# Performance work log

Measured on AMD Instinct MI355X. Metric: run time of the kernel, lower is better.

Reference implementation:

```python
import jax, jax.numpy as jnp
import numpy as np
from jax import lax

TIMESTEPS = 10
KSIZE = 2
STRIDE = 2


def setup_inputs() -> dict:
    key = jax.random.key(0)
    k1, _ = jax.random.split(key)
    x = jax.random.normal(k1, (32, 96, 128, 128), dtype=jnp.float32)
    # torch init: np.full((1, C, 1, 1), 0.1)
    pool_strength = jnp.ones((1, 96, 1, 1), dtype=jnp.float32) * 0.1
    return {"x": x, "pool_strength": pool_strength}


def _maxpool3x3_same(x):
    # MaxPool2d(kernel=3, stride=1, padding=1) on NCHW
    return lax.reduce_window(
        x, -jnp.inf, lax.max,
        window_dimensions=(1, 1, 3, 3),
        window_strides=(1, 1, 1, 1),
        padding=((0, 0), (0, 0), (1, 1), (1, 1)))


def reference(x, pool_strength):
    def step(cur, _):
        pooled = _maxpool3x3_same(cur)
        cur = cur + pool_strength * (pooled - cur)
        return cur, None

    cur, _ = lax.scan(step, x, None, length=TIMESTEPS)
    # AvgPool2d(kernel=2, stride=2, padding=0)
    s = lax.reduce_window(
        cur, 0.0, lax.add,
        window_dimensions=(1, 1, KSIZE, KSIZE),
        window_strides=(1, 1, STRIDE, STRIDE),
        padding='VALID')
    return s / float(KSIZE * KSIZE)
```

## Files before the change

kernel.cpp:

```cpp
#include <hip/hip_runtime.h>
#include <math.h>


#define TSTEPS 10
#define PW 128
#define PH 128
#define HPITCH 132

__device__ __forceinline__ float dpp_recv_left(float x) {
    int r = __builtin_amdgcn_update_dpp((int)0xff800000, __float_as_int(x),
                                        0x111, 0xf, 0xf, false);
    return __int_as_float(r);
}
__device__ __forceinline__ float dpp_recv_right(float x) {
    int r = __builtin_amdgcn_update_dpp((int)0xff800000, __float_as_int(x),
                                        0x101, 0xf, 0xf, false);
    return __int_as_float(r);
}

__device__ __forceinline__ float max3f(float a, float b, float c) {
    return fmaxf(fmaxf(a, b), c);
}

__device__ __forceinline__ void hmax_row(const float* v, float* h) {
    float vl = dpp_recv_left(v[7]);
    float vr = dpp_recv_right(v[0]);
    h[0] = max3f(vl, v[0], v[1]);
#pragma unroll
    for (int c = 1; c < 7; ++c) h[c] = max3f(v[c-1], v[c], v[c+1]);
    h[7] = max3f(v[6], v[7], vr);
}

__global__ __launch_bounds__(256, 3)
void cpool_kernel(const float* __restrict__ x, const float* __restrict__ ps,
                  float* __restrict__ out) {
    __shared__ float hbuf[32 * HPITCH];

    const int b  = blockIdx.x;
    const int ch = b % 96;
    const float p = ps[ch];

    const int tid = threadIdx.x;
    const int tx = tid & 15;
    const int ty = tid >> 4;
    const int x0 = tx << 3;
    const int y0 = ty << 3;

    const float* __restrict__ xp = x + (size_t)b * (PH * PW);

    float cur[8][8];
#pragma unroll
    for (int r = 0; r < 8; ++r) {
        const float4 a  = *(const float4*)(xp + (y0 + r) * PW + x0);
        const float4 bq = *(const float4*)(xp + (y0 + r) * PW + x0 + 4);
        cur[r][0] = a.x;  cur[r][1] = a.y;  cur[r][2] = a.z;  cur[r][3] = a.w;
        cur[r][4] = bq.x; cur[r][5] = bq.y; cur[r][6] = bq.z; cur[r][7] = bq.w;
    }

    const float NEG = -__builtin_huge_valf();

#pragma unroll 1
    for (int t = 0; t < TSTEPS; ++t) {
        float hTop[8], hBot[8];
        hmax_row(cur[0], hTop);
        hmax_row(cur[7], hBot);

        *(float4*)&hbuf[(2*ty)   * HPITCH + x0]     = make_float4(hTop[0], hTop[1], hTop[2], hTop[3]);
        *(float4*)&hbuf[(2*ty)   * HPITCH + x0 + 4] = make_float4(hTop[4], hTop[5], hTop[6], hTop[7]);
        *(float4*)&hbuf[(2*ty+1) * HPITCH + x0]     = make_float4(hBot[0], hBot[1], hBot[2], hBot[3]);
        *(float4*)&hbuf[(2*ty+1) * HPITCH + x0 + 4] = make_float4(hBot[4], hBot[5], hBot[6], hBot[7]);

        __syncthreads();

        float hm[8], hnx[8];
        if (ty > 0) {
            float4 a  = *(const float4*)&hbuf[(2*ty - 1) * HPITCH + x0];
            float4 bq = *(const float4*)&hbuf[(2*ty - 1) * HPITCH + x0 + 4];
            hm[0] = a.x;  hm[1] = a.y;  hm[2] = a.z;  hm[3] = a.w;
            hm[4] = bq.x; hm[5] = bq.y; hm[6] = bq.z; hm[7] = bq.w;
        } else {
#pragma unroll
            for (int c = 0; c < 8; ++c) hm[c] = NEG;
        }
        if (ty < 15) {
            float4 a  = *(const float4*)&hbuf[(2*ty + 2) * HPITCH + x0];
            float4 bq = *(const float4*)&hbuf[(2*ty + 2) * HPITCH + x0 + 4];
            hnx[0] = a.x;  hnx[1] = a.y;  hnx[2] = a.z;  hnx[3] = a.w;
            hnx[4] = bq.x; hnx[5] = bq.y; hnx[6] = bq.z; hnx[7] = bq.w;
        } else {
#pragma unroll
            for (int c = 0; c < 8; ++c) hnx[c] = NEG;
        }

        float hc[8];
#pragma unroll
        for (int c = 0; c < 8; ++c) hc[c] = hTop[c];

#pragma unroll
        for (int r = 0; r < 8; ++r) {
            float hn[8];
            if (r < 6) {
                hmax_row(cur[r + 1], hn);
            } else if (r == 6) {
#pragma unroll
                for (int c = 0; c < 8; ++c) hn[c] = hBot[c];
            } else {
#pragma unroll
                for (int c = 0; c < 8; ++c) hn[c] = hnx[c];
            }
#pragma unroll
            for (int c = 0; c < 8; ++c) {
                float v = max3f(hm[c], hc[c], hn[c]);
                cur[r][c] = fmaf(p, v - cur[r][c], cur[r][c]);
            }
#pragma unroll
            for (int c = 0; c < 8; ++c) { hm[c] = hc[c]; hc[c] = hn[c]; }
        }

        __syncthreads();
    }

    float* __restrict__ op = out + (size_t)b * (64 * 64);
#pragma unroll
    for (int r2 = 0; r2 < 4; ++r2) {
        float4 o;
        o.x = 0.25f * (cur[2*r2][0] + cur[2*r2][1] + cur[2*r2+1][0] + cur[2*r2+1][1]);
        o.y = 0.25f * (cur[2*r2][2] + cur[2*r2][3] + cur[2*r2+1][2] + cur[2*r2+1][3]);
        o.z = 0.25f * (cur[2*r2][4] + cur[2*r2][5] + cur[2*r2+1][4] + cur[2*r2+1][5]);
        o.w = 0.25f * (cur[2*r2][6] + cur[2*r2][7] + cur[2*r2+1][6] + cur[2*r2+1][7]);
        *(float4*)(op + (size_t)((ty * 4 + r2) * 64 + tx * 4)) = o;
    }
}

extern "C" void kernel_launch(void* const* d_in, const int* in_sizes, int n_in,
                              void* d_out, int out_size, void* d_ws, size_t ws_size,
                              hipStream_t stream) {
    const float* x  = (const float*)d_in[0];
    const float* ps = (const float*)d_in[1];
    float* out = (float*)d_out;
    (void)in_sizes; (void)n_in; (void)out_size; (void)d_ws; (void)ws_size;

    cpool_kernel<<<dim3(32 * 96), dim3(256), 0, stream>>>(x, ps, out);
}
```

Baseline: 300.0 us.

## Use 512 threads with 4x8 tiles and double-buffered halo exchange

```diff
diff --git a/kernel.cpp b/kernel.cpp
--- a/kernel.cpp
+++ b/kernel.cpp
@@ -1,18 +1,17 @@
 #include <hip/hip_runtime.h>
-#include <math.h>
 
 
 #define TSTEPS 10
 #define PW 128
-#define PH 128
-#define HPITCH 132
+#define HP 132
+#define HROWS 31
 
-__device__ __forceinline__ float dpp_recv_left(float x) {
+__device__ __forceinline__ float dpp_left(float x) {
     int r = __builtin_amdgcn_update_dpp((int)0xff800000, __float_as_int(x),
                                         0x111, 0xf, 0xf, false);
     return __int_as_float(r);
 }
-__device__ __forceinline__ float dpp_recv_right(float x) {
+__device__ __forceinline__ float dpp_right(float x) {
     int r = __builtin_amdgcn_update_dpp((int)0xff800000, __float_as_int(x),
                                         0x101, 0xf, 0xf, false);
     return __int_as_float(r);
@@ -23,112 +22,113 @@
 }
 
 __device__ __forceinline__ void hmax_row(const float* v, float* h) {
-    float vl = dpp_recv_left(v[7]);
-    float vr = dpp_recv_right(v[0]);
+    float vl = dpp_left(v[7]);
+    float vr = dpp_right(v[0]);
     h[0] = max3f(vl, v[0], v[1]);
 #pragma unroll
-    for (int c = 1; c < 7; ++c) h[c] = max3f(v[c-1], v[c], v[c+1]);
+    for (int c = 1; c < 7; ++c) h[c] = max3f(v[c - 1], v[c], v[c + 1]);
     h[7] = max3f(v[6], v[7], vr);
 }
 
-__global__ __launch_bounds__(256, 3)
+__device__ __forceinline__ void ld8(const float* a, float* d) {
+    float4 u = ((const float4*)a)[0], v = ((const float4*)a)[1];
+    d[0] = u.x; d[1] = u.y; d[2] = u.z; d[3] = u.w;
+    d[4] = v.x; d[5] = v.y; d[6] = v.z; d[7] = v.w;
+}
+__device__ __forceinline__ void st8(float* a, const float* d) {
+    ((float4*)a)[0] = make_float4(d[0], d[1], d[2], d[3]);
+    ((float4*)a)[1] = make_float4(d[4], d[5], d[6], d[7]);
+}
+
+__device__ __forceinline__ void do_step(float cur[4][8], float p, int tx, int ty,
+                                        float* __restrict__ topBuf,
+                                        float* __restrict__ botBuf) {
+    const float NEG = -__builtin_huge_valf();
+    const int x0 = tx * 8;
+
+    float hTop[8], hBot[8];
+    hmax_row(cur[0], hTop);
+    hmax_row(cur[3], hBot);
+
+    if (ty > 0)  st8(topBuf + (ty - 1) * HP + x0, hTop);
+    if (ty < 31) st8(botBuf + ty * HP + x0, hBot);
+
+    __syncthreads();
+
+    float hm[8], hnx[8];
+    if (ty > 0) {
+        ld8(botBuf + (ty - 1) * HP + x0, hm);
+    } else {
+#pragma unroll
+        for (int c = 0; c < 8; ++c) hm[c] = NEG;
+    }
+    if (ty < 31) {
+        ld8(topBuf + ty * HP + x0, hnx);
+    } else {
+#pragma unroll
+        for (int c = 0; c < 8; ++c) hnx[c] = NEG;
+    }
+
+    float hc[8];
+#pragma unroll
+    for (int c = 0; c < 8; ++c) hc[c] = hTop[c];
+
+#pragma unroll
+    for (int r = 0; r < 4; ++r) {
+        float hn[8];
+        if (r < 2) {
+            hmax_row(cur[r + 1], hn);
+        } else if (r == 2) {
+#pragma unroll
+            for (int c = 0; c < 8; ++c) hn[c] = hBot[c];
+        } else {
+#pragma unroll
+            for (int c = 0; c < 8; ++c) hn[c] = hnx[c];
+        }
+#pragma unroll
+        for (int c = 0; c < 8; ++c) {
+            float v = max3f(hm[c], hc[c], hn[c]);
+            cur[r][c] = fmaf(p, v - cur[r][c], cur[r][c]);
+        }
+#pragma unroll
+        for (int c = 0; c < 8; ++c) { hm[c] = hc[c]; hc[c] = hn[c]; }
+    }
+}
+
+__global__ __launch_bounds__(512, 4)
 void cpool_kernel(const float* __restrict__ x, const float* __restrict__ ps,
                   float* __restrict__ out) {
-    __shared__ float hbuf[32 * HPITCH];
+    __shared__ float lds[2][2][HROWS * HP];
 
-    const int b  = blockIdx.x;
-    const int ch = b % 96;
-    const float p = ps[ch];
+    const int b = blockIdx.x;
+    const float p = ps[b % 96];
 
-    const int tid = threadIdx.x;
-    const int tx = tid & 15;
-    const int ty = tid >> 4;
-    const int x0 = tx << 3;
-    const int y0 = ty << 3;
+    const int tx = threadIdx.x & 15;
+    const int ty = threadIdx.x >> 4;
+    const int x0 = tx * 8;
+    const int y0 = ty * 4;
 
-    const float* __restrict__ xp = x + (size_t)b * (PH * PW);
+    const float* __restrict__ xp = x + (size_t)b * (PW * PW);
 
-    float cur[8][8];
+    float cur[4][8];
 #pragma unroll
-    for (int r = 0; r < 8; ++r) {
-        const float4 a  = *(const float4*)(xp + (y0 + r) * PW + x0);
-        const float4 bq = *(const float4*)(xp + (y0 + r) * PW + x0 + 4);
-        cur[r][0] = a.x;  cur[r][1] = a.y;  cur[r][2] = a.z;  cur[r][3] = a.w;
-        cur[r][4] = bq.x; cur[r][5] = bq.y; cur[r][6] = bq.z; cur[r][7] = bq.w;
-    }
-
-    const float NEG = -__builtin_huge_valf();
+    for (int r = 0; r < 4; ++r) ld8(xp + (y0 + r) * PW + x0, cur[r]);
 
 #pragma unroll 1
-    for (int t = 0; t < TSTEPS; ++t) {
-        float hTop[8], hBot[8];
-        hmax_row(cur[0], hTop);
-        hmax_row(cur[7], hBot);
-
-        *(float4*)&hbuf[(2*ty)   * HPITCH + x0]     = make_float4(hTop[0], hTop[1], hTop[2], hTop[3]);
-        *(float4*)&hbuf[(2*ty)   * HPITCH + x0 + 4] = make_float4(hTop[4], hTop[5], hTop[6], hTop[7]);
-        *(float4*)&hbuf[(2*ty+1) * HPITCH + x0]     = make_float4(hBot[0], hBot[1], hBot[2], hBot[3]);
-        *(float4*)&hbuf[(2*ty+1) * HPITCH + x0 + 4] = make_float4(hBot[4], hBot[5], hBot[6], hBot[7]);
-
-        __syncthreads();
-
-        float hm[8], hnx[8];
-        if (ty > 0) {
-            float4 a  = *(const float4*)&hbuf[(2*ty - 1) * HPITCH + x0];
-            float4 bq = *(const float4*)&hbuf[(2*ty - 1) * HPITCH + x0 + 4];
-            hm[0] = a.x;  hm[1] = a.y;  hm[2] = a.z;  hm[3] = a.w;
-            hm[4] = bq.x; hm[5] = bq.y; hm[6] = bq.z; hm[7] = bq.w;
-        } else {
-#pragma unroll
-            for (int c = 0; c < 8; ++c) hm[c] = NEG;
-        }
-        if (ty < 15) {
-            float4 a  = *(const float4*)&hbuf[(2*ty + 2) * HPITCH + x0];
-            float4 bq = *(const float4*)&hbuf[(2*ty + 2) * HPITCH + x0 + 4];
-            hnx[0] = a.x;  hnx[1] = a.y;  hnx[2] = a.z;  hnx[3] = a.w;
-            hnx[4] = bq.x; hnx[5] = bq.y; hnx[6] = bq.z; hnx[7] = bq.w;
-        } else {
-#pragma unroll
-            for (int c = 0; c < 8; ++c) hnx[c] = NEG;
-        }
-
-        float hc[8];
-#pragma unroll
-        for (int c = 0; c < 8; ++c) hc[c] = hTop[c];
-
-#pragma unroll
-        for (int r = 0; r < 8; ++r) {
-            float hn[8];
-            if (r < 6) {
-                hmax_row(cur[r + 1], hn);
-            } else if (r == 6) {
-#pragma unroll
-                for (int c = 0; c < 8; ++c) hn[c] = hBot[c];
-            } else {
-#pragma unroll
-                for (int c = 0; c < 8; ++c) hn[c] = hnx[c];
-            }
-#pragma unroll
-            for (int c = 0; c < 8; ++c) {
-                float v = max3f(hm[c], hc[c], hn[c]);
-                cur[r][c] = fmaf(p, v - cur[r][c], cur[r][c]);
-            }
-#pragma unroll
-            for (int c = 0; c < 8; ++c) { hm[c] = hc[c]; hc[c] = hn[c]; }
-        }
-
-        __syncthreads();
+    for (int tt = 0; tt < TSTEPS / 2; ++tt) {
+        do_step(cur, p, tx, ty, lds[0][0], lds[0][1]);
+        do_step(cur, p, tx, ty, lds[1][0], lds[1][1]);
     }
 
     float* __restrict__ op = out + (size_t)b * (64 * 64);
 #pragma unroll
-    for (int r2 = 0; r2 < 4; ++r2) {
+    for (int r2 = 0; r2 < 2; ++r2) {
         float4 o;
         o.x = 0.25f * (cur[2*r2][0] + cur[2*r2][1] + cur[2*r2+1][0] + cur[2*r2+1][1]);
         o.y = 0.25f * (cur[2*r2][2] + cur[2*r2][3] + cur[2*r2+1][2] + cur[2*r2+1][3]);
         o.z = 0.25f * (cur[2*r2][4] + cur[2*r2][5] + cur[2*r2+1][4] + cur[2*r2+1][5]);
         o.w = 0.25f * (cur[2*r2][6] + cur[2*r2][7] + cur[2*r2+1][6] + cur[2*r2+1][7]);
-        *(float4*)(op + (size_t)((ty * 4 + r2) * 64 + tx * 4)) = o;
+        *(float4*)(op + (size_t)((2 * ty + r2) * 64 + tx * 4)) = o;
     }
 }
 
@@ -140,5 +140,5 @@
     float* out = (float*)d_out;
     (void)in_sizes; (void)n_in; (void)out_size; (void)d_ws; (void)ws_size;
 
-    cpool_kernel<<<dim3(32 * 96), dim3(256), 0, stream>>>(x, ps, out);
+    cpool_kernel<<<dim3(32 * 96), dim3(512), 0, stream>>>(x, ps, out);
 }
```

Result: faster. 292.9 us (-2.4%).

## Replace shared-memory halo exchange with per-wave redundant row bands

Applied to the files above, without the earlier changes.

```diff
diff --git a/kernel.cpp b/kernel.cpp
--- a/kernel.cpp
+++ b/kernel.cpp
@@ -1,20 +1,17 @@
 #include <hip/hip_runtime.h>
-#include <math.h>
 
 
+#define PW 128
 #define TSTEPS 10
-#define PW 128
-#define PH 128
-#define HPITCH 132
 
-__device__ __forceinline__ float dpp_recv_left(float x) {
+__device__ __forceinline__ float dpp_wave_left(float x) {
     int r = __builtin_amdgcn_update_dpp((int)0xff800000, __float_as_int(x),
-                                        0x111, 0xf, 0xf, false);
+                                        0x138, 0xf, 0xf, false);
     return __int_as_float(r);
 }
-__device__ __forceinline__ float dpp_recv_right(float x) {
+__device__ __forceinline__ float dpp_wave_right(float x) {
     int r = __builtin_amdgcn_update_dpp((int)0xff800000, __float_as_int(x),
-                                        0x101, 0xf, 0xf, false);
+                                        0x130, 0xf, 0xf, false);
     return __int_as_float(r);
 }
 
@@ -22,113 +19,78 @@
     return fmaxf(fmaxf(a, b), c);
 }
 
-__device__ __forceinline__ void hmax_row(const float* v, float* h) {
-    float vl = dpp_recv_left(v[7]);
-    float vr = dpp_recv_right(v[0]);
-    h[0] = max3f(vl, v[0], v[1]);
+template<int NROWS, int RS0>
+__device__ __forceinline__ void run_band(const float* __restrict__ xp,
+                                         float* __restrict__ op,
+                                         float p, int lane, int row_base,
+                                         int out_row0)
+{
+    float c0[NROWS], c1[NROWS];
+    const float* src = xp + (size_t)row_base * PW + 2 * lane;
 #pragma unroll
-    for (int c = 1; c < 7; ++c) h[c] = max3f(v[c-1], v[c], v[c+1]);
-    h[7] = max3f(v[6], v[7], vr);
-}
-
-__global__ __launch_bounds__(256, 3)
-void cpool_kernel(const float* __restrict__ x, const float* __restrict__ ps,
-                  float* __restrict__ out) {
-    __shared__ float hbuf[32 * HPITCH];
-
-    const int b  = blockIdx.x;
-    const int ch = b % 96;
-    const float p = ps[ch];
-
-    const int tid = threadIdx.x;
-    const int tx = tid & 15;
-    const int ty = tid >> 4;
-    const int x0 = tx << 3;
-    const int y0 = ty << 3;
-
-    const float* __restrict__ xp = x + (size_t)b * (PH * PW);
-
-    float cur[8][8];
-#pragma unroll
-    for (int r = 0; r < 8; ++r) {
-        const float4 a  = *(const float4*)(xp + (y0 + r) * PW + x0);
-        const float4 bq = *(const float4*)(xp + (y0 + r) * PW + x0 + 4);
-        cur[r][0] = a.x;  cur[r][1] = a.y;  cur[r][2] = a.z;  cur[r][3] = a.w;
-        cur[r][4] = bq.x; cur[r][5] = bq.y; cur[r][6] = bq.z; cur[r][7] = bq.w;
+    for (int rs = 0; rs < NROWS; ++rs) {
+        float2 v = *(const float2*)(src + rs * PW);
+        c0[rs] = v.x; c1[rs] = v.y;
     }
 
     const float NEG = -__builtin_huge_valf();
 
 #pragma unroll 1
     for (int t = 0; t < TSTEPS; ++t) {
-        float hTop[8], hBot[8];
-        hmax_row(cur[0], hTop);
-        hmax_row(cur[7], hBot);
-
-        *(float4*)&hbuf[(2*ty)   * HPITCH + x0]     = make_float4(hTop[0], hTop[1], hTop[2], hTop[3]);
-        *(float4*)&hbuf[(2*ty)   * HPITCH + x0 + 4] = make_float4(hTop[4], hTop[5], hTop[6], hTop[7]);
-        *(float4*)&hbuf[(2*ty+1) * HPITCH + x0]     = make_float4(hBot[0], hBot[1], hBot[2], hBot[3]);
-        *(float4*)&hbuf[(2*ty+1) * HPITCH + x0 + 4] = make_float4(hBot[4], hBot[5], hBot[6], hBot[7]);
-
-        __syncthreads();
-
-        float hm[8], hnx[8];
-        if (ty > 0) {
-            float4 a  = *(const float4*)&hbuf[(2*ty - 1) * HPITCH + x0];
-            float4 bq = *(const float4*)&hbuf[(2*ty - 1) * HPITCH + x0 + 4];
-            hm[0] = a.x;  hm[1] = a.y;  hm[2] = a.z;  hm[3] = a.w;
-            hm[4] = bq.x; hm[5] = bq.y; hm[6] = bq.z; hm[7] = bq.w;
-        } else {
+        float hp0 = NEG, hp1 = NEG;
+        float hc0, hc1;
+        {
+            float l = dpp_wave_left(c1[0]);
+            float r = dpp_wave_right(c0[0]);
+            hc0 = max3f(l, c0[0], c1[0]);
+            hc1 = max3f(c0[0], c1[0], r);
+        }
 #pragma unroll
-            for (int c = 0; c < 8; ++c) hm[c] = NEG;
+        for (int rs = 0; rs < NROWS; ++rs) {
+            float hn0, hn1;
+            if (rs < NROWS - 1) {
+                float l = dpp_wave_left(c1[rs + 1]);
+                float r = dpp_wave_right(c0[rs + 1]);
+                hn0 = max3f(l, c0[rs + 1], c1[rs + 1]);
+                hn1 = max3f(c0[rs + 1], c1[rs + 1], r);
+            } else {
+                hn0 = NEG; hn1 = NEG;
+            }
+            float v0 = max3f(hp0, hc0, hn0);
+            float v1 = max3f(hp1, hc1, hn1);
+            c0[rs] = fmaf(p, v0 - c0[rs], c0[rs]);
+            c1[rs] = fmaf(p, v1 - c1[rs], c1[rs]);
+            hp0 = hc0; hp1 = hc1; hc0 = hn0; hc1 = hn1;
         }
-        if (ty < 15) {
-            float4 a  = *(const float4*)&hbuf[(2*ty + 2) * HPITCH + x0];
-            float4 bq = *(const float4*)&hbuf[(2*ty + 2) * HPITCH + x0 + 4];
-            hnx[0] = a.x;  hnx[1] = a.y;  hnx[2] = a.z;  hnx[3] = a.w;
-            hnx[4] = bq.x; hnx[5] = bq.y; hnx[6] = bq.z; hnx[7] = bq.w;
-        } else {
-#pragma unroll
-            for (int c = 0; c < 8; ++c) hnx[c] = NEG;
-        }
-
-        float hc[8];
-#pragma unroll
-        for (int c = 0; c < 8; ++c) hc[c] = hTop[c];
+    }
 
 #pragma unroll
-        for (int r = 0; r < 8; ++r) {
-            float hn[8];
-            if (r < 6) {
-                hmax_row(cur[r + 1], hn);
-            } else if (r == 6) {
-#pragma unroll
-                for (int c = 0; c < 8; ++c) hn[c] = hBot[c];
-            } else {
-#pragma unroll
-                for (int c = 0; c < 8; ++c) hn[c] = hnx[c];
-            }
-#pragma unroll
-            for (int c = 0; c < 8; ++c) {
-                float v = max3f(hm[c], hc[c], hn[c]);
-                cur[r][c] = fmaf(p, v - cur[r][c], cur[r][c]);
-            }
-#pragma unroll
-            for (int c = 0; c < 8; ++c) { hm[c] = hc[c]; hc[c] = hn[c]; }
-        }
+    for (int j = 0; j < 16; ++j) {
+        const int rs = RS0 + 2 * j;
+        float o = 0.25f * (c0[rs] + c1[rs] + c0[rs + 1] + c1[rs + 1]);
+        op[(size_t)(out_row0 + j) * 64 + lane] = o;
+    }
+}
 
-        __syncthreads();
-    }
+__global__ __launch_bounds__(256, 3)
+void cpool_kernel(const float* __restrict__ x, const float* __restrict__ ps,
+                  float* __restrict__ out)
+{
+    const int b = blockIdx.x;
+    const float p = ps[b % 96];
+    const int lane = threadIdx.x & 63;
+    const int w = threadIdx.x >> 6;
 
-    float* __restrict__ op = out + (size_t)b * (64 * 64);
-#pragma unroll
-    for (int r2 = 0; r2 < 4; ++r2) {
-        float4 o;
-        o.x = 0.25f * (cur[2*r2][0] + cur[2*r2][1] + cur[2*r2+1][0] + cur[2*r2+1][1]);
-        o.y = 0.25f * (cur[2*r2][2] + cur[2*r2][3] + cur[2*r2+1][2] + cur[2*r2+1][3]);
-        o.z = 0.25f * (cur[2*r2][4] + cur[2*r2][5] + cur[2*r2+1][4] + cur[2*r2+1][5]);
-        o.w = 0.25f * (cur[2*r2][6] + cur[2*r2][7] + cur[2*r2+1][6] + cur[2*r2+1][7]);
-        *(float4*)(op + (size_t)((ty * 4 + r2) * 64 + tx * 4)) = o;
+    const float* xp = x + (size_t)b * (PW * PW);
+    float* op = out + (size_t)b * (64 * 64);
+
+    if (w == 0) {
+        run_band<42, 0>(xp, op, p, lane, 0, 0);
+    } else if (w == 3) {
+        run_band<42, 10>(xp, op, p, lane, 86, 48);
+    } else {
+        run_band<52, 10>(xp, op, p, lane, 32 * w - 10,
+                         16 * w);
     }
 }
 
```

Result: slower. 310.6 us (+3.5%).
